# Kernel tuning notes

Hardware: AMD Instinct MI355X
Metric: run time of the kernel (lower is better)

Reference implementation:

```python
import jax, jax.numpy as jnp
import numpy as np

ALPHA = 0.5
NUM_CLASSES = 86
FEAT = 256
N = 131072


def setup_inputs() -> dict:
    key = jax.random.key(0)
    k1, k2, k3 = jax.random.split(key, 3)
    features = jax.random.normal(k1, (N, FEAT), dtype=jnp.float32)
    labels = jax.random.randint(k2, (N,), 0, NUM_CLASSES)
    # non-trainable centers buffer, RandomNormal init (stddev 0.05 like keras default)
    centers = 0.05 * jax.random.normal(k3, (NUM_CLASSES, FEAT), dtype=jnp.float32)
    return {"features": features, "labels": labels, "centers": centers}


def reference(features, labels, centers):
    labels = labels.reshape(-1)
    # gather per-sample centers: [N, F]
    centers_batch = centers[labels]
    d = features - centers_batch
    # tf.nn.l2_loss = 0.5 * sum(x^2)
    loss = 0.5 * jnp.sum(d * d)
    # appear_times via unique_with_counts == per-class occurrence count gathered back
    counts = jax.ops.segment_sum(
        jnp.ones((labels.shape[0],), dtype=jnp.float32), labels,
        num_segments=NUM_CLASSES)  # [C]
    appear_times = counts[labels][:, None]  # [N, 1]
    diff = ALPHA * (-d) / (1.0 + appear_times)  # (centers_batch - features) scaled
    # tf.scatter_sub accumulates duplicate indices
    new_centers = centers.at[labels].add(-diff)
    return loss, new_centers
```

## Files before the change

kernel.cpp:

```cpp
#include <hip/hip_runtime.h>

#define ALPHA 0.5f
#define NCLS 86
#define FEAT 256
#define NTOT 131072

constexpr int K  = 64;
constexpr int CH = NTOT / K;
constexpr int L4 = CH / 4;

constexpr size_t WS_S   = 0;
constexpr size_t WS_CNT = (size_t)NCLS * K * FEAT;
constexpr size_t WS_L2  = WS_CNT + (size_t)NCLS * K;
constexpr size_t WS_CLS = WS_L2 + (size_t)NCLS * K;

__global__ __launch_bounds__(128) void ctc_main(
    const float4* __restrict__ feat4, const int4* __restrict__ lab4,
    float4* __restrict__ S_part4, float* __restrict__ cnt_part,
    float* __restrict__ l2_part)
{
    const int wave = threadIdx.x >> 6;
    const int lane = threadIdx.x & 63;
    const int pair = blockIdx.x * 2 + wave;
    const int k = pair % K;
    const int c = pair / K;
    const int base = k * CH;

    const int4* lp = lab4 + (base >> 2) + lane;
    const size_t dummy = (size_t)base * 64 + lane;

    float4 acc = {0.f, 0.f, 0.f, 0.f};
    float  acc2 = 0.f;
    int    cnt  = 0;

    int4 L = lp[0];
    for (int it = 0; it < L4; it += 64) {
        const int4 Lc = L;
        if (it + 64 < L4) L = lp[it + 64];
        unsigned long long m0 = __ballot(Lc.x == c);
        unsigned long long m1 = __ballot(Lc.y == c);
        unsigned long long m2 = __ballot(Lc.z == c);
        unsigned long long m3 = __ballot(Lc.w == c);
        cnt += __popcll(m0) + __popcll(m1) + __popcll(m2) + __popcll(m3);

#define ACCUM(v)                                                           \
        { acc.x += v.x; acc.y += v.y; acc.z += v.z; acc.w += v.w;          \
          acc2  += v.x * v.x + v.y * v.y + v.z * v.z + v.w * v.w; }
        while (m0 | m1 | m2 | m3) {
            const bool h0 = m0 != 0, h1 = m1 != 0, h2 = m2 != 0, h3 = m3 != 0;
            const int b0 = (int)__ffsll((long long)m0) - 1;
            const int b1 = (int)__ffsll((long long)m1) - 1;
            const int b2 = (int)__ffsll((long long)m2) - 1;
            const int b3 = (int)__ffsll((long long)m3) - 1;
            m0 &= m0 - 1; m1 &= m1 - 1; m2 &= m2 - 1; m3 &= m3 - 1;
            const float4 v0 = feat4[h0 ? (size_t)(base + (it + b0) * 4 + 0) * 64 + lane : dummy];
            const float4 v1 = feat4[h1 ? (size_t)(base + (it + b1) * 4 + 1) * 64 + lane : dummy];
            const float4 v2 = feat4[h2 ? (size_t)(base + (it + b2) * 4 + 2) * 64 + lane : dummy];
            const float4 v3 = feat4[h3 ? (size_t)(base + (it + b3) * 4 + 3) * 64 + lane : dummy];
            if (h0) ACCUM(v0)
            if (h1) ACCUM(v1)
            if (h2) ACCUM(v2)
            if (h3) ACCUM(v3)
        }
#undef ACCUM
    }

    S_part4[(size_t)pair * 64 + lane] = acc;

    for (int off = 32; off; off >>= 1)
        acc2 += __shfl_down(acc2, off, 64);
    if (lane == 0) {
        cnt_part[pair] = (float)cnt;
        l2_part[pair]  = acc2;
    }
}

__global__ __launch_bounds__(1024) void ctc_finalize(
    const float* __restrict__ centers, const float* __restrict__ S_part,
    const float* __restrict__ cnt_part, const float* __restrict__ l2_part,
    float* __restrict__ class_loss, float* __restrict__ out_centers)
{
    const int c  = blockIdx.x;
    const int t  = threadIdx.x & 255;
    const int kq = threadIdx.x >> 8;

    float S = 0.f;
#pragma unroll
    for (int j = 0; j < 16; ++j)
        S += S_part[((size_t)c * K + kq * 16 + j) * FEAT + t];

    __shared__ float red[4][FEAT];
    __shared__ float r2[4];
    __shared__ float sn_s, sl2_s;
    red[kq][t] = S;

    if (threadIdx.x < 64) {
        float a = cnt_part[c * K + threadIdx.x];
        float b = l2_part[c * K + threadIdx.x];
        for (int off = 32; off; off >>= 1) {
            a += __shfl_down(a, off, 64);
            b += __shfl_down(b, off, 64);
        }
        if (threadIdx.x == 0) { sn_s = a; sl2_s = b; }
    }
    __syncthreads();

    if (threadIdx.x < 256) {
        const float Sf = red[0][t] + red[1][t] + red[2][t] + red[3][t];
        const float n  = sn_s;
        const float cc = centers[c * FEAT + t];
        out_centers[c * FEAT + t] = cc + ALPHA * (Sf - n * cc) / (1.f + n);
        float part = 0.5f * n * cc * cc - Sf * cc;
        for (int off = 32; off; off >>= 1) part += __shfl_down(part, off, 64);
        if ((t & 63) == 0) r2[t >> 6] = part;
    }
    __syncthreads();
    if (threadIdx.x == 0)
        class_loss[c] = r2[0] + r2[1] + r2[2] + r2[3] + 0.5f * sl2_s;
}

__global__ void ctc_loss_write(const float* __restrict__ class_loss,
                               float* __restrict__ out)
{
    const int l = threadIdx.x;
    float v = (l < NCLS) ? class_loss[l] : 0.f;
    if (l + 64 < NCLS) v += class_loss[l + 64];
    for (int off = 32; off; off >>= 1) v += __shfl_down(v, off, 64);
    if (l == 0) out[0] = v;
}

extern "C" void kernel_launch(void* const* d_in, const int* in_sizes, int n_in,
                              void* d_out, int out_size, void* d_ws, size_t ws_size,
                              hipStream_t stream)
{
    const float* feat    = (const float*)d_in[0];
    const int*   labels  = (const int*)d_in[1];
    const float* centers = (const float*)d_in[2];
    float* out = (float*)d_out;
    float* ws  = (float*)d_ws;

    float* S_part     = ws + WS_S;
    float* cnt_part   = ws + WS_CNT;
    float* l2_part    = ws + WS_L2;
    float* class_loss = ws + WS_CLS;

    ctc_main<<<NCLS * K / 2, 128, 0, stream>>>(
        (const float4*)feat, (const int4*)labels,
        (float4*)S_part, cnt_part, l2_part);

    ctc_finalize<<<NCLS, 1024, 0, stream>>>(
        centers, S_part, cnt_part, l2_part, class_loss, out + 1);

    ctc_loss_write<<<1, 64, 0, stream>>>(class_loss, out);
}
```

Baseline: 32.68 us.

## Double per-class chunk split and fold final loss reduction into finalize via atomics

Raises the number of label chunks per class from 64 to 128, doubling the grid of the main scan kernel so more waves run in parallel and each scans half as many labels. It removes the third single-block loss kernel by having each finalize block atomically add its class loss and letting the last-arriving block write the total. The counters are reset inside the main kernel. This adds float atomic nondeterminism, doubles the partial-sum workspace the finalize kernel must read, and saves one kernel launch.

Result: slower. 34.34 us (+5.1%).

```diff
diff --git a/kernel.cpp b/kernel.cpp
--- a/kernel.cpp
+++ b/kernel.cpp
@@ -5,24 +5,28 @@
 #define FEAT 256
 #define NTOT 131072
 
-constexpr int K  = 64;
+constexpr int K  = 128;
 constexpr int CH = NTOT / K;
 constexpr int L4 = CH / 4;
 
-constexpr size_t WS_S   = 0;
-constexpr size_t WS_CNT = (size_t)NCLS * K * FEAT;
-constexpr size_t WS_L2  = WS_CNT + (size_t)NCLS * K;
-constexpr size_t WS_CLS = WS_L2 + (size_t)NCLS * K;
+constexpr size_t WS_S    = 0;
+constexpr size_t WS_CNT  = (size_t)NCLS * K * FEAT;
+constexpr size_t WS_L2   = WS_CNT + (size_t)NCLS * K;
+constexpr size_t WS_LOSS = WS_L2 + (size_t)NCLS * K;
+constexpr size_t WS_DONE = WS_LOSS + 1;
 
 __global__ __launch_bounds__(128) void ctc_main(
     const float4* __restrict__ feat4, const int4* __restrict__ lab4,
     float4* __restrict__ S_part4, float* __restrict__ cnt_part,
-    float* __restrict__ l2_part)
+    float* __restrict__ l2_part, float* __restrict__ loss_acc,
+    int* __restrict__ done)
 {
+    if (threadIdx.x == 0) { *loss_acc = 0.f; *done = 0; }
+
     const int wave = threadIdx.x >> 6;
     const int lane = threadIdx.x & 63;
     const int pair = blockIdx.x * 2 + wave;
-    const int k = pair % K;
+    const int k = pair & (K - 1);
     const int c = pair / K;
     const int base = k * CH;
 
@@ -78,7 +82,8 @@
 __global__ __launch_bounds__(1024) void ctc_finalize(
     const float* __restrict__ centers, const float* __restrict__ S_part,
     const float* __restrict__ cnt_part, const float* __restrict__ l2_part,
-    float* __restrict__ class_loss, float* __restrict__ out_centers)
+    float* __restrict__ loss_acc, int* __restrict__ done,
+    float* __restrict__ out)
 {
     const int c  = blockIdx.x;
     const int t  = threadIdx.x & 255;
@@ -86,8 +91,8 @@
 
     float S = 0.f;
 #pragma unroll
-    for (int j = 0; j < 16; ++j)
-        S += S_part[((size_t)c * K + kq * 16 + j) * FEAT + t];
+    for (int j = 0; j < K / 4; ++j)
+        S += S_part[((size_t)c * K + kq * (K / 4) + j) * FEAT + t];
 
     __shared__ float red[4][FEAT];
     __shared__ float r2[4];
@@ -95,8 +100,8 @@
     red[kq][t] = S;
 
     if (threadIdx.x < 64) {
-        float a = cnt_part[c * K + threadIdx.x];
-        float b = l2_part[c * K + threadIdx.x];
+        float a = cnt_part[c * K + threadIdx.x] + cnt_part[c * K + 64 + threadIdx.x];
+        float b = l2_part[c * K + threadIdx.x]  + l2_part[c * K + 64 + threadIdx.x];
         for (int off = 32; off; off >>= 1) {
             a += __shfl_down(a, off, 64);
             b += __shfl_down(b, off, 64);
@@ -109,24 +114,22 @@
         const float Sf = red[0][t] + red[1][t] + red[2][t] + red[3][t];
         const float n  = sn_s;
         const float cc = centers[c * FEAT + t];
-        out_centers[c * FEAT + t] = cc + ALPHA * (Sf - n * cc) / (1.f + n);
+        out[1 + c * FEAT + t] = cc + ALPHA * (Sf - n * cc) / (1.f + n);
         float part = 0.5f * n * cc * cc - Sf * cc;
         for (int off = 32; off; off >>= 1) part += __shfl_down(part, off, 64);
         if ((t & 63) == 0) r2[t >> 6] = part;
     }
     __syncthreads();
-    if (threadIdx.x == 0)
-        class_loss[c] = r2[0] + r2[1] + r2[2] + r2[3] + 0.5f * sl2_s;
-}
 
-__global__ void ctc_loss_write(const float* __restrict__ class_loss,
-                               float* __restrict__ out)
-{
-    const int l = threadIdx.x;
-    float v = (l < NCLS) ? class_loss[l] : 0.f;
-    if (l + 64 < NCLS) v += class_loss[l + 64];
-    for (int off = 32; off; off >>= 1) v += __shfl_down(v, off, 64);
-    if (l == 0) out[0] = v;
+    if (threadIdx.x == 0) {
+        const float my = r2[0] + r2[1] + r2[2] + r2[3] + 0.5f * sl2_s;
+        atomicAdd(loss_acc, my);
+        __threadfence();
+        const int old = atomicAdd(done, 1);
+        if (old == NCLS - 1) {
+            out[0] = atomicAdd(loss_acc, 0.f);
+        }
+    }
 }
 
 extern "C" void kernel_launch(void* const* d_in, const int* in_sizes, int n_in,
@@ -139,17 +142,16 @@
     float* out = (float*)d_out;
     float* ws  = (float*)d_ws;
 
-    float* S_part     = ws + WS_S;
-    float* cnt_part   = ws + WS_CNT;
-    float* l2_part    = ws + WS_L2;
-    float* class_loss = ws + WS_CLS;
+    float* S_part   = ws + WS_S;
+    float* cnt_part = ws + WS_CNT;
+    float* l2_part  = ws + WS_L2;
+    float* loss_acc = ws + WS_LOSS;
+    int*   done     = (int*)(ws + WS_DONE);
 
     ctc_main<<<NCLS * K / 2, 128, 0, stream>>>(
         (const float4*)feat, (const int4*)labels,
-        (float4*)S_part, cnt_part, l2_part);
+        (float4*)S_part, cnt_part, l2_part, loss_acc, done);
 
     ctc_finalize<<<NCLS, 1024, 0, stream>>>(
-        centers, S_part, cnt_part, l2_part, class_loss, out + 1);
-
-    ctc_loss_write<<<1, 64, 0, stream>>>(class_loss, out);
+        centers, S_part, cnt_part, l2_part, loss_acc, done, out);
 }
```
